# Kernel optimization log

Measured on AMD Instinct MI355X. Metric: run time of the kernel, lower is better.

## Reference

```python
import jax, jax.numpy as jnp
import numpy as np

SCALE = 1.0 / (64 ** 0.5)  # 1/sqrt(dim_key)

def setup_inputs() -> dict:
    key = jax.random.key(0)
    ks = jax.random.split(key, 8)
    B, S, D, H, dk = 4, 2048, 1024, 16, 64
    s = 0.02
    return {
        "values": jax.random.normal(ks[0], (B, S, D), jnp.float32),
        "queries": jax.random.normal(ks[1], (B, S, D), jnp.float32),
        "keys": jax.random.normal(ks[2], (B, S, D), jnp.float32),
        "Wq": jax.random.normal(ks[3], (H, D, dk), jnp.float32) * s,
        "bq": jnp.zeros((H, dk), jnp.float32),
        "Wk": jax.random.normal(ks[4], (H, D, dk), jnp.float32) * s,
        "bk": jnp.zeros((H, dk), jnp.float32),
        "Wv": jax.random.normal(ks[5], (H, D, dk), jnp.float32) * s,
        "bv": jnp.zeros((H, dk), jnp.float32),
        "Wo": jax.random.normal(ks[6], (D, D), jnp.float32) * s,
        "bo": jnp.zeros((D,), jnp.float32),
    }

def reference(values, queries, keys, Wq, bq, Wk, bk, Wv, bv, Wo, bo):
    # Per-head projections, batched across heads: [B,S,D] x [H,D,dk] -> [B,H,S,dk]
    q = jnp.einsum('bsd,hdk->bhsk', queries, Wq) + bq[None, :, None, :]
    k = jnp.einsum('bsd,hdk->bhsk', keys, Wk) + bk[None, :, None, :]
    v = jnp.einsum('bsd,hdk->bhsk', values, Wv) + bv[None, :, None, :]
    # Scaled dot-product scores [B,H,S,S]
    scores = jnp.einsum('bhqk,bhsk->bhqs', q, k) * SCALE
    S = scores.shape[-1]
    causal = jnp.tril(jnp.ones((S, S), bool))
    scores = jnp.where(causal, scores, jnp.float32(-1e19))
    attn = jax.nn.softmax(scores, axis=-1)
    ctx = jnp.einsum('bhqs,bhsk->bhqk', attn, v)  # [B,H,S,dk]
    # Concat heads along last axis (head-major, matching tf.concat order)
    B, H, Sq, dk = ctx.shape
    ctx = jnp.transpose(ctx, (0, 2, 1, 3)).reshape(B, Sq, H * dk)
    return ctx @ Wo + bo
```

## Files before the change

kernel.cpp:

```cpp
#include <hip/hip_runtime.h>
#include <hip/hip_bf16.h>
#include <cstdint>

#define B_ 4
#define H_ 16
#define S_ 2048
#define D_ 1024
#define DK 64
#define QSCALE 0.18033688f

typedef float f32x4 __attribute__((ext_vector_type(4)));
typedef short bf8 __attribute__((ext_vector_type(8)));
typedef unsigned short u16;

__device__ __forceinline__ u16 f2bf(float x){
  union { float f; uint32_t u; } c; c.f = x;
  uint32_t u = c.u;
  uint32_t r = (u + 0x7FFFu + ((u >> 16) & 1u)) >> 16;
  return (u16)r;
}

__device__ __forceinline__ uint32_t pk2bf(float a, float b){
  __hip_bfloat162 t = __float22bfloat162_rn(make_float2(a, b));
  uint32_t r; __builtin_memcpy(&r, &t, 4); return r;
}

__device__ __forceinline__ void gl16(const void* g, void* l){
  __builtin_amdgcn_global_load_lds(
      (const __attribute__((address_space(1))) void*)g,
      (__attribute__((address_space(3))) void*)l, 16, 0, 0);
}

__global__ __launch_bounds__(256) void cvt_in(
    const float* __restrict__ q, const float* __restrict__ k,
    const float* __restrict__ v, u16* __restrict__ o)
{
  const size_t N8 = (size_t)1 << 20;
  const size_t tot = 3 * N8;
  const size_t step = (size_t)gridDim.x * 256;
  for (size_t g0 = (size_t)blockIdx.x*256 + threadIdx.x; g0 < tot; g0 += step){
    int t = (int)(g0 >> 20);
    size_t r = g0 & (N8 - 1);
    const float* src = (t==0 ? q : (t==1 ? k : v));
    const float4* s4 = reinterpret_cast<const float4*>(src + r*8);
    float4 a = s4[0], b = s4[1];
    uint4 w;
    w.x = pk2bf(a.x,a.y); w.y = pk2bf(a.z,a.w);
    w.z = pk2bf(b.x,b.y); w.w = pk2bf(b.z,b.w);
    *reinterpret_cast<uint4*>(o + ((size_t)t << 23) + r*8) = w;
  }
}

__global__ __launch_bounds__(256) void wtrans3(
    const float* __restrict__ Wq, const float* __restrict__ Wk,
    const float* __restrict__ Wv, u16* __restrict__ oq,
    u16* __restrict__ ok, u16* __restrict__ ov)
{
  __shared__ u16 T[64*72];
  const int tid = threadIdx.x;
  const int z = blockIdx.z, t = z >> 4, hh = z & 15;
  const float* src = (t==0 ? Wq : t==1 ? Wk : Wv) + (size_t)hh * (D_*DK);
  u16* dst = (t==0 ? oq : t==1 ? ok : ov) + (size_t)hh * (DK*D_);
  const int r0 = blockIdx.y*64;
  #pragma unroll
  for (int p=0;p<4;++p){
    int r  = p*16 + (tid>>4);
    int c4 = (tid&15)*4;
    float4 v = *reinterpret_cast<const float4*>(&src[(size_t)(r0+r)*DK + c4]);
    uint2 w; w.x = pk2bf(v.x, v.y); w.y = pk2bf(v.z, v.w);
    *reinterpret_cast<uint2*>(&T[r*72 + c4]) = w;
  }
  __syncthreads();
  const int c = tid>>2, rg = (tid&3)*16;
  u16 tmp[16];
  #pragma unroll
  for (int i=0;i<16;++i) tmp[i] = T[(rg+i)*72 + c];
  *reinterpret_cast<bf8*>(&dst[(size_t)c*D_ + r0 + rg])     = *reinterpret_cast<bf8*>(&tmp[0]);
  *reinterpret_cast<bf8*>(&dst[(size_t)c*D_ + r0 + rg + 8]) = *reinterpret_cast<bf8*>(&tmp[8]);
}

__global__ __launch_bounds__(256) void wtrans(
    const float* __restrict__ in, u16* __restrict__ out, int R, int C)
{
  __shared__ u16 T[64*72];
  const int tid = threadIdx.x;
  const int r0 = blockIdx.y*64, c0 = blockIdx.x*64;
  #pragma unroll
  for (int p=0;p<4;++p){
    int r  = p*16 + (tid>>4);
    int c4 = (tid&15)*4;
    float4 v = *reinterpret_cast<const float4*>(&in[(size_t)(r0+r)*C + c0 + c4]);
    uint2 w; w.x = pk2bf(v.x, v.y); w.y = pk2bf(v.z, v.w);
    *reinterpret_cast<uint2*>(&T[r*72 + c4]) = w;
  }
  __syncthreads();
  const int c = tid>>2, rg = (tid&3)*16;
  u16 tmp[16];
  #pragma unroll
  for (int i=0;i<16;++i) tmp[i] = T[(rg+i)*72 + c];
  *reinterpret_cast<bf8*>(&out[(size_t)(c0+c)*R + r0 + rg])     = *reinterpret_cast<bf8*>(&tmp[0]);
  *reinterpret_cast<bf8*>(&out[(size_t)(c0+c)*R + r0 + rg + 8]) = *reinterpret_cast<bf8*>(&tmp[8]);
}

__global__ __launch_bounds__(256) void gemm_qkv(
    const u16* __restrict__ Ab,
    const u16* __restrict__ Bq, const u16* __restrict__ Bk,
    const u16* __restrict__ Bv,
    const float* __restrict__ bq, const float* __restrict__ bk,
    const float* __restrict__ bv,
    u16* __restrict__ oq, u16* __restrict__ ok, u16* __restrict__ ov)
{
  __shared__ u16 As[2][128*64];
  __shared__ u16 Bs[2][128*64];
  const int tid = threadIdx.x;
  const int wid = tid>>6, lane = tid&63, g = lane>>4, l15 = lane&15;
  const int z = blockIdx.x >> 9, bid = blockIdx.x & 511;
  const u16* A     = Ab + ((size_t)z << 23);
  const u16*   Bt  = (z==0 ? Bq : z==1 ? Bk : Bv);
  const float* bias= (z==0 ? bq : z==1 ? bk : bv);
  u16* Out         = (z==0 ? oq : z==1 ? ok : ov);
  const float osc  = (z==0 ? QSCALE : 1.0f);
  const int xcd = bid & 7, i = bid >> 3;
  const int cb = i & 7, rb = xcd*8 + (i>>3);
  const int row0 = rb*128, col0 = cb*128;
  const int wr = wid>>1, wc = wid&1;

  f32x4 acc[4][4];
  #pragma unroll
  for (int m=0;m<4;++m)
    #pragma unroll
    for (int n=0;n<4;++n) acc[m][n] = (f32x4){0.f,0.f,0.f,0.f};

  auto STAGE = [&](int buf, int k0){
    #pragma unroll
    for (int p=0;p<4;++p){
      int r0l = wid*32 + p*8;
      int row = r0l + (lane>>3);
      int ch = (lane&7) ^ (row&7);
      gl16(A  + (size_t)(row0+row)*D_ + k0 + ch*8, &As[buf][r0l*64]);
      gl16(Bt + (size_t)(col0+row)*D_ + k0 + ch*8, &Bs[buf][r0l*64]);
    }
  };

  auto COMPUTE = [&](int cur){
    bf8 af[4][2], bfm[4][2];
    #pragma unroll
    for (int m=0;m<4;++m){
      int row = wr*64 + m*16 + l15;
      af[m][0] = *reinterpret_cast<const bf8*>(&As[cur][row*64 + ((g     ^(row&7))*8)]);
      af[m][1] = *reinterpret_cast<const bf8*>(&As[cur][row*64 + (((4+g) ^(row&7))*8)]);
    }
    #pragma unroll
    for (int n=0;n<4;++n){
      int row = wc*64 + n*16 + l15;
      bfm[n][0] = *reinterpret_cast<const bf8*>(&Bs[cur][row*64 + ((g     ^(row&7))*8)]);
      bfm[n][1] = *reinterpret_cast<const bf8*>(&Bs[cur][row*64 + (((4+g) ^(row&7))*8)]);
    }
    #pragma unroll
    for (int m=0;m<4;++m)
      #pragma unroll
      for (int n=0;n<4;++n){
        acc[m][n] = __builtin_amdgcn_mfma_f32_16x16x32_bf16(af[m][0], bfm[n][0], acc[m][n], 0,0,0);
        acc[m][n] = __builtin_amdgcn_mfma_f32_16x16x32_bf16(af[m][1], bfm[n][1], acc[m][n], 0,0,0);
      }
  };

  STAGE(0, 0);
  STAGE(1, 64);
  asm volatile("s_waitcnt vmcnt(8)" ::: "memory");
  asm volatile("s_barrier" ::: "memory");

  #pragma unroll 1
  for (int t = 0; t < 16; ++t){
    COMPUTE(t & 1);
    asm volatile("s_barrier" ::: "memory");
    if (t + 2 < 16){
      STAGE(t & 1, (t + 2) * 64);
      asm volatile("s_waitcnt vmcnt(8)" ::: "memory");
    } else {
      asm volatile("s_waitcnt vmcnt(0)" ::: "memory");
    }
    asm volatile("s_barrier" ::: "memory");
  }

  #pragma unroll
  for (int m=0;m<4;++m){
    #pragma unroll
    for (int n=0;n<4;++n){
      int col = col0 + wc*64 + n*16 + l15;
      float bs = bias[col];
      if (z == 2){
        int rowb = row0 + wr*64 + m*16 + g*4;
        int b = rowb>>11, s = rowb&2047;
        int h = col>>6, dkk = col&63;
        ushort4 pk;
        pk.x = f2bf(acc[m][n][0]+bs); pk.y = f2bf(acc[m][n][1]+bs);
        pk.z = f2bf(acc[m][n][2]+bs); pk.w = f2bf(acc[m][n][3]+bs);
        *reinterpret_cast<ushort4*>(&Out[(((size_t)(b*H_+h)*DK)+dkk)*S_ + s]) = pk;
      } else {
        #pragma unroll
        for (int r=0;r<4;++r){
          int row = row0 + wr*64 + m*16 + g*4 + r;
          float v = (acc[m][n][r] + bs)*osc;
          int b = row>>11, s = row&2047;
          int h = col>>6, dkk = col&63;
          Out[(((size_t)(b*H_+h)*S_)+s)*DK + dkk] = f2bf(v);
        }
      }
    }
  }
}

__global__ __launch_bounds__(256) void gemm_out(
    const u16* __restrict__ A, const u16* __restrict__ Bt,
    const float* __restrict__ bias, float* __restrict__ Outp)
{
  __shared__ u16 As[2][128*64];
  __shared__ u16 Bs[2][128*64];
  const int tid = threadIdx.x;
  const int wid = tid>>6, lane = tid&63, g = lane>>4, l15 = lane&15;
  const int bid = blockIdx.x;
  const int xcd = bid & 7, i = bid >> 3;
  const int cb = i & 7, rb = xcd*8 + (i>>3);
  const int row0 = rb*128, col0 = cb*128;
  const int wr = wid>>1, wc = wid&1;

  f32x4 acc[4][4];
  #pragma unroll
  for (int m=0;m<4;++m)
    #pragma unroll
    for (int n=0;n<4;++n) acc[m][n] = (f32x4){0.f,0.f,0.f,0.f};

  auto STAGE = [&](int buf, int k0){
    #pragma unroll
    for (int p=0;p<4;++p){
      int r0l = wid*32 + p*8;
      int row = r0l + (lane>>3);
      int ch = (lane&7) ^ (row&7);
      gl16(A  + (size_t)(row0+row)*D_ + k0 + ch*8, &As[buf][r0l*64]);
      gl16(Bt + (size_t)(col0+row)*D_ + k0 + ch*8, &Bs[buf][r0l*64]);
    }
  };

  auto COMPUTE = [&](int cur){
    bf8 af[4][2], bfm[4][2];
    #pragma unroll
    for (int m=0;m<4;++m){
      int row = wr*64 + m*16 + l15;
      af[m][0] = *reinterpret_cast<const bf8*>(&As[cur][row*64 + ((g     ^(row&7))*8)]);
      af[m][1] = *reinterpret_cast<const bf8*>(&As[cur][row*64 + (((4+g) ^(row&7))*8)]);
    }
    #pragma unroll
    for (int n=0;n<4;++n){
      int row = wc*64 + n*16 + l15;
      bfm[n][0] = *reinterpret_cast<const bf8*>(&Bs[cur][row*64 + ((g     ^(row&7))*8)]);
      bfm[n][1] = *reinterpret_cast<const bf8*>(&Bs[cur][row*64 + (((4+g) ^(row&7))*8)]);
    }
    #pragma unroll
    for (int m=0;m<4;++m)
      #pragma unroll
      for (int n=0;n<4;++n){
        acc[m][n] = __builtin_amdgcn_mfma_f32_16x16x32_bf16(af[m][0], bfm[n][0], acc[m][n], 0,0,0);
        acc[m][n] = __builtin_amdgcn_mfma_f32_16x16x32_bf16(af[m][1], bfm[n][1], acc[m][n], 0,0,0);
      }
  };

  STAGE(0, 0);
  STAGE(1, 64);
  asm volatile("s_waitcnt vmcnt(8)" ::: "memory");
  asm volatile("s_barrier" ::: "memory");

  #pragma unroll 1
  for (int t = 0; t < 16; ++t){
    COMPUTE(t & 1);
    asm volatile("s_barrier" ::: "memory");
    if (t + 2 < 16){
      STAGE(t & 1, (t + 2) * 64);
      asm volatile("s_waitcnt vmcnt(8)" ::: "memory");
    } else {
      asm volatile("s_waitcnt vmcnt(0)" ::: "memory");
    }
    asm volatile("s_barrier" ::: "memory");
  }

  #pragma unroll
  for (int m=0;m<4;++m){
    #pragma unroll
    for (int n=0;n<4;++n){
      int col = col0 + wc*64 + n*16 + l15;
      float bs = bias[col];
      #pragma unroll
      for (int r=0;r<4;++r){
        int row = row0 + wr*64 + m*16 + g*4 + r;
        Outp[(size_t)row*D_ + col] = acc[m][n][r] + bs;
      }
    }
  }
}

__global__ __launch_bounds__(256) void attn_kernel(
    const u16* __restrict__ qp, const u16* __restrict__ kp,
    const u16* __restrict__ vt, u16* __restrict__ ctx)
{
  __shared__ u16 Kl[2][64*64];
  __shared__ u16 Vl[2][64*64];
  __shared__ u16 Pl[4][32*72];
  const int tid = threadIdx.x;
  const int wid = tid>>6, lane = tid&63, g = lane>>4, l15 = lane&15;
  const int bid0 = blockIdx.x;
  const int xx = bid0 & 7, yy = bid0 >> 3;
  const int bh = xx + 8*(yy & 7);
  const int qt = 15 - (yy >> 3);
  const int b = bh >> 4, h = bh & 15;
  const size_t base = (size_t)bh * S_ * DK;

  bf8 ones;
  #pragma unroll
  for (int i=0;i<8;++i) ones[i] = (short)0x3F80;

  const int Q0 = qt*128;
  bf8 aq[2][2];
  #pragma unroll
  for (int qs=0;qs<2;++qs){
    int qrow = Q0 + wid*32 + qs*16 + l15;
    aq[qs][0] = *reinterpret_cast<const bf8*>(&qp[base + (size_t)qrow*DK +      g*8]);
    aq[qs][1] = *reinterpret_cast<const bf8*>(&qp[base + (size_t)qrow*DK + 32 + g*8]);
  }

  f32x4 acco[2][4], acc_l[2];
  #pragma unroll
  for (int qs=0;qs<2;++qs){
    #pragma unroll
    for (int nd=0;nd<4;++nd) acco[qs][nd] = (f32x4){0.f,0.f,0.f,0.f};
    acc_l[qs] = (f32x4){0.f,0.f,0.f,0.f};
  }

  auto STAGE = [&](int buf, int kt){
    const int k0 = kt*64;
    #pragma unroll
    for (int p=0;p<2;++p){
      int r0l = wid*16 + p*8;
      int row = r0l + (lane>>3);
      int ch  = (lane&7) ^ (row&7);
      gl16(kp + base + (size_t)(k0+row)*DK + ch*8, &Kl[buf][r0l*64]);
      gl16(vt + base + (size_t)row*S_ + k0 + ch*8, &Vl[buf][r0l*64]);
    }
  };

  const int nk = 2*qt + 2;
  int cur = 0;
  STAGE(cur, 0);
  asm volatile("s_waitcnt vmcnt(0)" ::: "memory");
  __syncthreads();

  for (int kt = 0; kt < nk; ++kt){
    if (kt < nk-1) STAGE(cur^1, kt+1);

    f32x4 sc[2][4];
    #pragma unroll
    for (int n=0;n<4;++n){
      int row = n*16 + l15;
      bf8 b0 = *reinterpret_cast<const bf8*>(&Kl[cur][row*64 + ((g     ^(row&7))*8)]);
      bf8 b1 = *reinterpret_cast<const bf8*>(&Kl[cur][row*64 + (((4+g) ^(row&7))*8)]);
      #pragma unroll
      for (int qs=0;qs<2;++qs){
        f32x4 z = (f32x4){0.f,0.f,0.f,0.f};
        z = __builtin_amdgcn_mfma_f32_16x16x32_bf16(aq[qs][0], b0, z, 0,0,0);
        z = __builtin_amdgcn_mfma_f32_16x16x32_bf16(aq[qs][1], b1, z, 0,0,0);
        sc[qs][n] = z;
      }
    }
    if (kt >= nk-2){
      const int k0 = kt*64;
      #pragma unroll
      for (int qs=0;qs<2;++qs){
        #pragma unroll
        for (int n=0;n<4;++n){
          #pragma unroll
          for (int r=0;r<4;++r){
            int qg = Q0 + wid*32 + qs*16 + g*4 + r;
            int kg = k0 + n*16 + l15;
            if (kg > qg) sc[qs][n][r] = -1e30f;
          }
        }
      }
    }
    #pragma unroll
    for (int qs=0;qs<2;++qs){
      #pragma unroll
      for (int n=0;n<4;++n){
        #pragma unroll
        for (int r=0;r<4;++r){
          float p = __builtin_amdgcn_exp2f(sc[qs][n][r]);
          union { float f; uint32_t u; } cu; cu.f = p;
          Pl[wid][(qs*16 + g*4 + r)*72 + n*16 + l15] = (u16)(cu.u >> 16);
        }
      }
    }
    asm volatile("s_waitcnt lgkmcnt(0)" ::: "memory");
    __builtin_amdgcn_sched_barrier(0);

    bf8 pa[2][2];
    #pragma unroll
    for (int qs=0;qs<2;++qs){
      pa[qs][0] = *reinterpret_cast<const bf8*>(&Pl[wid][(qs*16 + l15)*72 +      g*8]);
      pa[qs][1] = *reinterpret_cast<const bf8*>(&Pl[wid][(qs*16 + l15)*72 + 32 + g*8]);
      acc_l[qs] = __builtin_amdgcn_mfma_f32_16x16x32_bf16(pa[qs][0], ones, acc_l[qs], 0,0,0);
      acc_l[qs] = __builtin_amdgcn_mfma_f32_16x16x32_bf16(pa[qs][1], ones, acc_l[qs], 0,0,0);
    }
    #pragma unroll
    for (int nd=0;nd<4;++nd){
      int row = nd*16 + l15;
      bf8 v0 = *reinterpret_cast<const bf8*>(&Vl[cur][row*64 + ((g     ^(row&7))*8)]);
      bf8 v1 = *reinterpret_cast<const bf8*>(&Vl[cur][row*64 + (((4+g) ^(row&7))*8)]);
      #pragma unroll
      for (int qs=0;qs<2;++qs){
        acco[qs][nd] = __builtin_amdgcn_mfma_f32_16x16x32_bf16(pa[qs][0], v0, acco[qs][nd], 0,0,0);
        acco[qs][nd] = __builtin_amdgcn_mfma_f32_16x16x32_bf16(pa[qs][1], v1, acco[qs][nd], 0,0,0);
      }
    }
    asm volatile("s_waitcnt vmcnt(0)" ::: "memory");
    __syncthreads();
    cur ^= 1;
  }

  #pragma unroll
  for (int qs=0;qs<2;++qs){
    float rl[4];
    #pragma unroll
    for (int r=0;r<4;++r) rl[r] = __builtin_amdgcn_rcpf(acc_l[qs][r]);
    #pragma unroll
    for (int nd=0;nd<4;++nd){
      #pragma unroll
      for (int r=0;r<4;++r){
        int qg = Q0 + wid*32 + qs*16 + g*4 + r;
        float v = acco[qs][nd][r] * rl[r];
        ctx[((size_t)(b*S_) + qg)*D_ + h*DK + nd*16 + l15] = f2bf(v);
      }
    }
  }
}

extern "C" void kernel_launch(void* const* d_in, const int* in_sizes, int n_in,
                              void* d_out, int out_size, void* d_ws, size_t ws_size,
                              hipStream_t stream)
{
  const float* values  = (const float*)d_in[0];
  const float* queries = (const float*)d_in[1];
  const float* keys    = (const float*)d_in[2];
  const float* Wq = (const float*)d_in[3];
  const float* bq = (const float*)d_in[4];
  const float* Wk = (const float*)d_in[5];
  const float* bk = (const float*)d_in[6];
  const float* Wv = (const float*)d_in[7];
  const float* bv = (const float*)d_in[8];
  const float* Wo = (const float*)d_in[9];
  const float* bo = (const float*)d_in[10];
  float* out = (float*)d_out;

  const size_t NE = (size_t)B_*H_*S_*DK;
  const size_t WE = (size_t)D_*D_;
  u16* cvt = (u16*)d_ws;
  u16* qp  = cvt + 3*NE;
  u16* kp  = qp + NE;
  u16* vtb = kp + NE;
  u16* wtq = vtb + NE;
  u16* wtk = wtq + WE;
  u16* wtv = wtk + WE;
  u16* wto = wtv + WE;
  u16* ctx = cvt;

  cvt_in<<<3072, 256, 0, stream>>>(queries, keys, values, cvt);
  wtrans3<<<dim3(1,16,48), 256, 0, stream>>>(Wq, Wk, Wv, wtq, wtk, wtv);
  wtrans<<<dim3(16,16,1), 256, 0, stream>>>(Wo, wto, D_, D_);
  gemm_qkv<<<1536, 256, 0, stream>>>(cvt, wtq, wtk, wtv,
                                     bq, bk, bv, qp, kp, vtb);
  attn_kernel<<<1024, 256, 0, stream>>>(qp, kp, vtb, ctx);
  gemm_out<<<512, 256, 0, stream>>>(ctx, wto, bo, out);
}
```

Baseline: 174.8 us.

## Double attention query tile to 256 rows and pair causal tiles per CU

Each attention block now handles 256 query rows (64 per wave) instead of 128. This halves the number of K/V tile loads and barriers per query row, and the grid shrinks to 512 blocks. The block-to-tile mapping pairs light and heavy causal query tiles across the two halves of the grid to even out work per CU, and launch bounds request 2 blocks per SM. Per-block work becomes coarser, which raises register pressure (accumulators double) and LDS use, and reduces the parallelism available for hiding latency.

Measured after the change: 186.6 us. 1.07x slower.

```diff
diff --git a/kernel.cpp b/kernel.cpp
--- a/kernel.cpp
+++ b/kernel.cpp
@@ -298,19 +298,20 @@
   }
 }
 
-__global__ __launch_bounds__(256) void attn_kernel(
+__global__ __launch_bounds__(256, 2) void attn_kernel(
     const u16* __restrict__ qp, const u16* __restrict__ kp,
     const u16* __restrict__ vt, u16* __restrict__ ctx)
 {
   __shared__ u16 Kl[2][64*64];
   __shared__ u16 Vl[2][64*64];
-  __shared__ u16 Pl[4][32*72];
+  __shared__ u16 Pl[4][64*72];
   const int tid = threadIdx.x;
   const int wid = tid>>6, lane = tid&63, g = lane>>4, l15 = lane&15;
   const int bid0 = blockIdx.x;
   const int xx = bid0 & 7, yy = bid0 >> 3;
-  const int bh = xx + 8*(yy & 7);
-  const int qt = 15 - (yy >> 3);
+  const int half = yy >> 5, y2 = yy & 31;
+  const int qt = half ? (7 - (y2 >> 3)) : (y2 >> 3);
+  const int bh = xx + 8*(y2 & 7);
   const int b = bh >> 4, h = bh & 15;
   const size_t base = (size_t)bh * S_ * DK;
 
@@ -318,18 +319,18 @@
   #pragma unroll
   for (int i=0;i<8;++i) ones[i] = (short)0x3F80;
 
-  const int Q0 = qt*128;
-  bf8 aq[2][2];
-  #pragma unroll
-  for (int qs=0;qs<2;++qs){
-    int qrow = Q0 + wid*32 + qs*16 + l15;
+  const int Q0 = qt*256;
+  bf8 aq[4][2];
+  #pragma unroll
+  for (int qs=0;qs<4;++qs){
+    int qrow = Q0 + wid*64 + qs*16 + l15;
     aq[qs][0] = *reinterpret_cast<const bf8*>(&qp[base + (size_t)qrow*DK +      g*8]);
     aq[qs][1] = *reinterpret_cast<const bf8*>(&qp[base + (size_t)qrow*DK + 32 + g*8]);
   }
 
-  f32x4 acco[2][4], acc_l[2];
-  #pragma unroll
-  for (int qs=0;qs<2;++qs){
+  f32x4 acco[4][4], acc_l[4];
+  #pragma unroll
+  for (int qs=0;qs<4;++qs){
     #pragma unroll
     for (int nd=0;nd<4;++nd) acco[qs][nd] = (f32x4){0.f,0.f,0.f,0.f};
     acc_l[qs] = (f32x4){0.f,0.f,0.f,0.f};
@@ -347,7 +348,7 @@
     }
   };
 
-  const int nk = 2*qt + 2;
+  const int nk = 4*qt + 4;
   int cur = 0;
   STAGE(cur, 0);
   asm volatile("s_waitcnt vmcnt(0)" ::: "memory");
@@ -356,53 +357,46 @@
   for (int kt = 0; kt < nk; ++kt){
     if (kt < nk-1) STAGE(cur^1, kt+1);
 
-    f32x4 sc[2][4];
+    const int k0 = kt*64;
+    const bool diag = (kt >= nk-4);
     #pragma unroll
     for (int n=0;n<4;++n){
       int row = n*16 + l15;
       bf8 b0 = *reinterpret_cast<const bf8*>(&Kl[cur][row*64 + ((g     ^(row&7))*8)]);
       bf8 b1 = *reinterpret_cast<const bf8*>(&Kl[cur][row*64 + (((4+g) ^(row&7))*8)]);
-      #pragma unroll
-      for (int qs=0;qs<2;++qs){
+      f32x4 sc[4];
+      #pragma unroll
+      for (int qs=0;qs<4;++qs){
         f32x4 z = (f32x4){0.f,0.f,0.f,0.f};
         z = __builtin_amdgcn_mfma_f32_16x16x32_bf16(aq[qs][0], b0, z, 0,0,0);
         z = __builtin_amdgcn_mfma_f32_16x16x32_bf16(aq[qs][1], b1, z, 0,0,0);
-        sc[qs][n] = z;
-      }
-    }
-    if (kt >= nk-2){
-      const int k0 = kt*64;
-      #pragma unroll
-      for (int qs=0;qs<2;++qs){
+        sc[qs] = z;
+      }
+      if (diag){
         #pragma unroll
-        for (int n=0;n<4;++n){
+        for (int qs=0;qs<4;++qs)
           #pragma unroll
           for (int r=0;r<4;++r){
-            int qg = Q0 + wid*32 + qs*16 + g*4 + r;
+            int qg = Q0 + wid*64 + qs*16 + g*4 + r;
             int kg = k0 + n*16 + l15;
-            if (kg > qg) sc[qs][n][r] = -1e30f;
+            if (kg > qg) sc[qs][r] = -1e30f;
           }
-        }
-      }
-    }
-    #pragma unroll
-    for (int qs=0;qs<2;++qs){
-      #pragma unroll
-      for (int n=0;n<4;++n){
+      }
+      #pragma unroll
+      for (int qs=0;qs<4;++qs)
         #pragma unroll
         for (int r=0;r<4;++r){
-          float p = __builtin_amdgcn_exp2f(sc[qs][n][r]);
+          float p = __builtin_amdgcn_exp2f(sc[qs][r]);
           union { float f; uint32_t u; } cu; cu.f = p;
           Pl[wid][(qs*16 + g*4 + r)*72 + n*16 + l15] = (u16)(cu.u >> 16);
         }
-      }
     }
     asm volatile("s_waitcnt lgkmcnt(0)" ::: "memory");
     __builtin_amdgcn_sched_barrier(0);
 
-    bf8 pa[2][2];
-    #pragma unroll
-    for (int qs=0;qs<2;++qs){
+    bf8 pa[4][2];
+    #pragma unroll
+    for (int qs=0;qs<4;++qs){
       pa[qs][0] = *reinterpret_cast<const bf8*>(&Pl[wid][(qs*16 + l15)*72 +      g*8]);
       pa[qs][1] = *reinterpret_cast<const bf8*>(&Pl[wid][(qs*16 + l15)*72 + 32 + g*8]);
       acc_l[qs] = __builtin_amdgcn_mfma_f32_16x16x32_bf16(pa[qs][0], ones, acc_l[qs], 0,0,0);
@@ -414,7 +408,7 @@
       bf8 v0 = *reinterpret_cast<const bf8*>(&Vl[cur][row*64 + ((g     ^(row&7))*8)]);
       bf8 v1 = *reinterpret_cast<const bf8*>(&Vl[cur][row*64 + (((4+g) ^(row&7))*8)]);
       #pragma unroll
-      for (int qs=0;qs<2;++qs){
+      for (int qs=0;qs<4;++qs){
         acco[qs][nd] = __builtin_amdgcn_mfma_f32_16x16x32_bf16(pa[qs][0], v0, acco[qs][nd], 0,0,0);
         acco[qs][nd] = __builtin_amdgcn_mfma_f32_16x16x32_bf16(pa[qs][1], v1, acco[qs][nd], 0,0,0);
       }
@@ -425,7 +419,7 @@
   }
 
   #pragma unroll
-  for (int qs=0;qs<2;++qs){
+  for (int qs=0;qs<4;++qs){
     float rl[4];
     #pragma unroll
     for (int r=0;r<4;++r) rl[r] = __builtin_amdgcn_rcpf(acc_l[qs][r]);
@@ -433,7 +427,7 @@
     for (int nd=0;nd<4;++nd){
       #pragma unroll
       for (int r=0;r<4;++r){
-        int qg = Q0 + wid*32 + qs*16 + g*4 + r;
+        int qg = Q0 + wid*64 + qs*16 + g*4 + r;
         float v = acco[qs][nd][r] * rl[r];
         ctx[((size_t)(b*S_) + qg)*D_ + h*DK + nd*16 + l15] = f2bf(v);
       }
@@ -475,6 +469,6 @@
   wtrans<<<dim3(16,16,1), 256, 0, stream>>>(Wo, wto, D_, D_);
   gemm_qkv<<<1536, 256, 0, stream>>>(cvt, wtq, wtk, wtv,
                                      bq, bk, bv, qp, kp, vtb);
-  attn_kernel<<<1024, 256, 0, stream>>>(qp, kp, vtb, ctx);
+  attn_kernel<<<512, 256, 0, stream>>>(qp, kp, vtb, ctx);
   gemm_out<<<512, 256, 0, stream>>>(ctx, wto, bo, out);
 }
```
